# Performance work log

Measured on AMD Instinct MI355X. Metric: run time of the kernel, lower is better.

## Reference

```python
import jax, jax.numpy as jnp
import numpy as np
import math

WIDTH = 1024
NUM_HEADS = 16
HEAD_DIM = WIDTH // NUM_HEADS
WINDOW_SIZE = 256
MIN_LOGITS_VALUE = -1e30


def setup_inputs() -> dict:
    key = jax.random.key(0)
    ks = jax.random.split(key, 7)
    b, t = 2, 2048
    std = math.sqrt(1.0 / WIDTH)
    x = jax.random.normal(ks[0], (b, t, WIDTH), dtype=jnp.float32)
    segment_pos = jnp.broadcast_to(jnp.arange(t, dtype=jnp.int32)[None, :], (b, t))
    Wq = jax.random.normal(ks[1], (WIDTH, WIDTH), dtype=jnp.float32) * std
    Wk = jax.random.normal(ks[2], (HEAD_DIM, WIDTH), dtype=jnp.float32) * std
    Wv = jax.random.normal(ks[3], (HEAD_DIM, WIDTH), dtype=jnp.float32) * std
    Wf = jax.random.normal(ks[4], (WIDTH, WIDTH), dtype=jnp.float32) * std
    bf = jnp.zeros((WIDTH,), dtype=jnp.float32)
    return {"x": x, "segment_pos": segment_pos, "Wq": Wq, "Wk": Wk, "Wv": Wv, "Wf": Wf, "bf": bf}


def reference(x, segment_pos, Wq, Wk, Wv, Wf, bf):
    b, t, _ = x.shape
    # projections (Linear: x @ W.T)
    q = (x @ Wq.T).reshape(b, t, NUM_HEADS, HEAD_DIM)  # [b,t,n,h]
    k = x @ Wk.T  # [b,t,h] single shared KV head (MQA)
    v = x @ Wv.T  # [b,t,h]
    scale = 1.0 / math.sqrt(HEAD_DIM)
    logits = jnp.einsum('btnh,bsh->bnts', q, k) * scale  # [b,n,t,s]
    # sliding-window causal mask: q_pos >= k_pos and q_pos <= k_pos + window
    ar = jnp.arange(t)
    qp = ar[:, None]
    kp = ar[None, :]
    mask = (qp >= kp) & (qp <= kp + WINDOW_SIZE)  # [t,s]
    masked = jnp.where(mask[None, None, :, :], logits, MIN_LOGITS_VALUE)
    probs = jax.nn.softmax(masked.astype(jnp.float32), axis=-1).astype(logits.dtype)
    out = jnp.einsum('bnts,bsh->btnh', probs, v)  # [b,t,n,h]
    out = out.reshape(b, t, WIDTH)
    return out @ Wf.T + bf
```

## Files before the change

kernel.cpp:

```cpp
#include <hip/hip_runtime.h>
#include <stdint.h>

#define B_SZ   2
#define T_SEQ  2048
#define WIDTH_ 1024
#define NH     16
#define HD     64
#define WIN    256
#define MROWS  (B_SZ * T_SEQ)
#define NQKV   1152

typedef __attribute__((ext_vector_type(4))) float f32x4;
typedef __attribute__((ext_vector_type(8))) short s16x8;

typedef __attribute__((address_space(1))) const void gas_void;
typedef __attribute__((address_space(3))) void las_void;

#define MFMA(a, b, c) __builtin_amdgcn_mfma_f32_16x16x32_bf16((a), (b), (c), 0, 0, 0)

__device__ __forceinline__ void gload_lds16(const void* g, void* l) {
  __builtin_amdgcn_global_load_lds((gas_void*)g, (las_void*)l, 16, 0, 0);
}

__device__ __forceinline__ ushort f2bf(float f) {
  union { float f; uint32_t u; } v; v.f = f;
  uint32_t u = v.u;
  return (ushort)((u + 0x7FFFu + ((u >> 16) & 1u)) >> 16);
}

__global__ void prep_kernel(const float* __restrict__ x,
                            const float* __restrict__ Wq,
                            const float* __restrict__ Wk,
                            const float* __restrict__ Wv,
                            const float* __restrict__ Wf,
                            ushort* __restrict__ xb,
                            ushort* __restrict__ wqkv,
                            ushort* __restrict__ wfb) {
  const int XN = MROWS * WIDTH_ / 4;
  const int WQ = NQKV * WIDTH_ / 4;
  const int WF = WIDTH_ * WIDTH_ / 4;
  int i = blockIdx.x * blockDim.x + threadIdx.x;
  float4 v;
  ushort* dst;
  if (i < XN) {
    v = ((const float4*)x)[i];
    dst = xb + i * 4;
  } else if (i < XN + WQ) {
    int j = i - XN;
    int row = (j * 4) >> 10;
    int col = (j * 4) & 1023;
    const float* src = (row < 1024) ? (Wq + row * 1024 + col)
                     : (row < 1088) ? (Wk + (row - 1024) * 1024 + col)
                                    : (Wv + (row - 1088) * 1024 + col);
    v = *(const float4*)src;
    dst = wqkv + j * 4;
  } else if (i < XN + WQ + WF) {
    int j = i - XN - WQ;
    v = ((const float4*)Wf)[j];
    dst = wfb + j * 4;
  } else {
    return;
  }
  ushort4 o;
  o.x = f2bf(v.x); o.y = f2bf(v.y); o.z = f2bf(v.z); o.w = f2bf(v.w);
  *(ushort4*)dst = o;
}

template <int MODE>
__global__ __launch_bounds__(256) void gemm_kernel(
    const ushort* __restrict__ A, const ushort* __restrict__ B,
    ushort* __restrict__ qb, ushort* __restrict__ kb, ushort* __restrict__ vb,
    float* __restrict__ Cf, const float* __restrict__ bias) {
  const int K = 1024;
  const int w = threadIdx.x >> 6;
  const int lane = threadIdx.x & 63;
  const int g = lane >> 4;
  const int r16 = lane & 15;
  const int m0 = blockIdx.y * 128;
  const int n0 = blockIdx.x * 128;
  const int wm = (w >> 1) * 64;
  const int wn = (w & 1) * 64;

  __shared__ ushort As[128 * 32];
  __shared__ ushort Bs[128 * 32];

  f32x4 acc[4][4] = {};

  for (int k0 = 0; k0 < K; k0 += 32) {
#pragma unroll
    for (int i = 0; i < 2; ++i) {
      int c = i * 256 + w * 64 + lane;
      int row = c >> 2;
      int ke = (c & 3) * 8;
      int ldsbase = (i * 256 + w * 64) * 16;
      gload_lds16(A + (size_t)(m0 + row) * K + k0 + ke, (char*)As + ldsbase);
      gload_lds16(B + (size_t)(n0 + row) * K + k0 + ke, (char*)Bs + ldsbase);
    }
    __syncthreads();

    s16x8 af[4], bfr[4];
#pragma unroll
    for (int t = 0; t < 4; ++t) {
      af[t]  = *(const s16x8*)&As[(wm + t * 16 + r16) * 32 + g * 8];
      bfr[t] = *(const s16x8*)&Bs[(wn + t * 16 + r16) * 32 + g * 8];
    }
#pragma unroll
    for (int mb = 0; mb < 4; ++mb)
#pragma unroll
      for (int nb = 0; nb < 4; ++nb)
        acc[mb][nb] = MFMA(af[mb], bfr[nb], acc[mb][nb]);
    __syncthreads();
  }

#pragma unroll
  for (int mb = 0; mb < 4; ++mb)
#pragma unroll
    for (int nb = 0; nb < 4; ++nb) {
      int n = n0 + wn + nb * 16 + r16;
      int mbase = m0 + wm + mb * 16 + 4 * g;
      if (MODE == 0) {
#pragma unroll
        for (int r = 0; r < 4; ++r) {
          ushort h = f2bf(acc[mb][nb][r]);
          int m = mbase + r;
          if (n < 1024)      qb[m * 1024 + n] = h;
          else if (n < 1088) kb[m * 64 + (n - 1024)] = h;
          else               vb[m * 64 + (n - 1088)] = h;
        }
      } else {
        float bv = bias[n];
#pragma unroll
        for (int r = 0; r < 4; ++r)
          Cf[(size_t)(mbase + r) * 1024 + n] = acc[mb][nb][r] + bv;
      }
    }
}

__global__ void vtrans_kernel(const ushort* __restrict__ vb,
                              ushort* __restrict__ vt) {
  int o = blockIdx.x * blockDim.x + threadIdx.x;
  int t = o & 2047;
  int d = (o >> 11) & 63;
  int b = o >> 17;
  vt[o] = vb[(size_t)(b * 2048 + t) * 64 + d];
}

__global__ __launch_bounds__(64) void attn_kernel(
    const ushort* __restrict__ qb, const ushort* __restrict__ kb,
    const ushort* __restrict__ vt, ushort* __restrict__ ao) {
  const int lane = threadIdx.x;
  const int g = lane >> 4;
  const int r16 = lane & 15;
  const int blk = blockIdx.x;
  const int qt = blk & 127;
  const int h = (blk >> 7) & 15;
  const int b = blk >> 11;
  const int q0 = qt * 16;
  const int qp = q0 + r16;

  const ushort* qrow = qb + (size_t)(b * 2048 + qp) * 1024 + h * 64;
  s16x8 qf0 = *(const s16x8*)(qrow + g * 8);
  s16x8 qf1 = *(const s16x8*)(qrow + 32 + g * 8);

  f32x4 oacc[4] = {};
  float mrun = -1e30f, ls = 0.f;

  int kt0 = q0 - WIN;
  if (kt0 < 0) kt0 = 0;
  kt0 &= ~31;

  for (int kt = kt0; kt <= q0; kt += 32) {
    int kr0 = kt + r16;
    int kr1 = kt + 16 + r16;
    if (kr1 > 2047) kr1 = 2047;
    const ushort* kp0 = kb + (size_t)(b * 2048 + kr0) * 64;
    const ushort* kp1 = kb + (size_t)(b * 2048 + kr1) * 64;
    s16x8 k00 = *(const s16x8*)(kp0 + g * 8);
    s16x8 k01 = *(const s16x8*)(kp0 + 32 + g * 8);
    s16x8 k10 = *(const s16x8*)(kp1 + g * 8);
    s16x8 k11 = *(const s16x8*)(kp1 + 32 + g * 8);

    f32x4 s0 = {}, s1 = {};
    s0 = MFMA(k00, qf0, s0);
    s0 = MFMA(k01, qf1, s0);
    s1 = MFMA(k10, qf0, s1);
    s1 = MFMA(k11, qf1, s1);

    float p0[4], p1[4];
    float tm = -1e30f;
#pragma unroll
    for (int r = 0; r < 4; ++r) {
      int ka = kt + 4 * g + r;
      int kb2 = ka + 16;
      float v0 = (ka <= qp && qp - ka <= WIN) ? s0[r] * 0.125f : -1e30f;
      float v1 = (kb2 <= qp && qp - kb2 <= WIN) ? s1[r] * 0.125f : -1e30f;
      p0[r] = v0; p1[r] = v1;
      tm = fmaxf(tm, fmaxf(v0, v1));
    }
    tm = fmaxf(tm, __shfl_xor(tm, 16));
    tm = fmaxf(tm, __shfl_xor(tm, 32));

    float mnew = fmaxf(mrun, tm);
    float corr = __expf(mrun - mnew);
    float ts = 0.f;
    s16x8 pf;
#pragma unroll
    for (int r = 0; r < 4; ++r) {
      float e0 = __expf(p0[r] - mnew);
      float e1 = __expf(p1[r] - mnew);
      ts += e0 + e1;
      pf[r] = (short)f2bf(e0);
      pf[4 + r] = (short)f2bf(e1);
    }
    ts += __shfl_xor(ts, 16);
    ts += __shfl_xor(ts, 32);
    ls = ls * corr + ts;
    mrun = mnew;

#pragma unroll
    for (int db = 0; db < 4; ++db) oacc[db] *= corr;

#pragma unroll
    for (int db = 0; db < 4; ++db) {
      const ushort* vrow = vt + (size_t)(b * 64 + db * 16 + r16) * 2048 + kt;
      ushort4 va = *(const ushort4*)(vrow + 4 * g);
      ushort4 vc = *(const ushort4*)(vrow + 16 + 4 * g);
      s16x8 vf;
      vf[0] = (short)va.x; vf[1] = (short)va.y; vf[2] = (short)va.z; vf[3] = (short)va.w;
      vf[4] = (short)vc.x; vf[5] = (short)vc.y; vf[6] = (short)vc.z; vf[7] = (short)vc.w;
      oacc[db] = MFMA(vf, pf, oacc[db]);
    }
  }

  float inv = 1.0f / ls;
  ushort* orow = ao + (size_t)(b * 2048 + qp) * 1024 + h * 64;
#pragma unroll
  for (int db = 0; db < 4; ++db) {
    ushort4 o;
    o.x = f2bf(oacc[db][0] * inv);
    o.y = f2bf(oacc[db][1] * inv);
    o.z = f2bf(oacc[db][2] * inv);
    o.w = f2bf(oacc[db][3] * inv);
    *(ushort4*)(orow + db * 16 + 4 * g) = o;
  }
}

extern "C" void kernel_launch(void* const* d_in, const int* in_sizes, int n_in,
                              void* d_out, int out_size, void* d_ws, size_t ws_size,
                              hipStream_t stream) {
  const float* x  = (const float*)d_in[0];
  const float* Wq = (const float*)d_in[2];
  const float* Wk = (const float*)d_in[3];
  const float* Wv = (const float*)d_in[4];
  const float* Wf = (const float*)d_in[5];
  const float* bf = (const float*)d_in[6];
  float* out = (float*)d_out;

  uint8_t* w8 = (uint8_t*)d_ws;
  ushort* xb   = (ushort*)(w8 + 0);
  ushort* qbuf = (ushort*)(w8 + 8388608);
  ushort* attn = (ushort*)(w8 + 16777216);
  ushort* wqkv = (ushort*)(w8 + 25165824);
  ushort* wfb  = (ushort*)(w8 + 27525120);
  ushort* vt   = (ushort*)(w8 + 29622272);
  ushort* kbuf = (ushort*)(w8 + 30146560);
  ushort* vbuf = (ushort*)(w8 + 30670848);

  prep_kernel<<<6272, 256, 0, stream>>>(x, Wq, Wk, Wv, Wf, xb, wqkv, wfb);
  gemm_kernel<0><<<dim3(9, 32), 256, 0, stream>>>(xb, wqkv, qbuf, kbuf, vbuf,
                                                  nullptr, nullptr);
  vtrans_kernel<<<1024, 256, 0, stream>>>(vbuf, vt);
  attn_kernel<<<4096, 64, 0, stream>>>(qbuf, kbuf, vt, attn);
  gemm_kernel<1><<<dim3(8, 32), 256, 0, stream>>>(attn, wfb, nullptr, nullptr,
                                                  nullptr, out, bf);
}
```

Before: 187.0 us.

## Double-buffer GEMM LDS, fuse V transpose into epilogue, widen attention to 32 queries

The GEMM kernel now double-buffers its LDS tiles, so the global-to-LDS loads for the next K slice are issued while the current slice is being computed. The QKV GEMM epilogue writes V directly in transposed layout, which removes the separate vtrans kernel launch and its extra pass over V. Each attention block now handles 32 queries instead of 16, so K and V fragments loaded once are shared across two query groups, and the next K tile is prefetched into registers. In exchange, LDS use doubles, attention register pressure rises, the transposed V stores in the epilogue are strided, and the attention grid is halved, which lowers occupancy.

```diff
diff --git a/kernel.cpp b/kernel.cpp
--- a/kernel.cpp
+++ b/kernel.cpp
@@ -66,12 +66,39 @@
   *(ushort4*)dst = o;
 }
 
+#define G_STAGE(AS, BS, KOFF) do {                                          \
+  _Pragma("unroll")                                                         \
+  for (int i_ = 0; i_ < 2; ++i_) {                                          \
+    int c_ = i_ * 256 + w * 64 + lane;                                      \
+    int row_ = c_ >> 2;                                                     \
+    int ke_ = (c_ & 3) * 8;                                                 \
+    int ldsb_ = (i_ * 256 + w * 64) * 16;                                   \
+    gload_lds16(A + (size_t)(m0 + row_) * 1024 + (KOFF) + ke_,              \
+                (char*)(AS) + ldsb_);                                       \
+    gload_lds16(B + (size_t)(n0 + row_) * 1024 + (KOFF) + ke_,              \
+                (char*)(BS) + ldsb_);                                       \
+  }                                                                         \
+} while (0)
+
+#define G_COMPUTE(AS, BS) do {                                              \
+  s16x8 af_[4], bf_[4];                                                     \
+  _Pragma("unroll")                                                         \
+  for (int t_ = 0; t_ < 4; ++t_) {                                          \
+    af_[t_] = *(const s16x8*)&(AS)[(wm + t_ * 16 + r16) * 32 + g * 8];      \
+    bf_[t_] = *(const s16x8*)&(BS)[(wn + t_ * 16 + r16) * 32 + g * 8];      \
+  }                                                                         \
+  _Pragma("unroll")                                                         \
+  for (int mb_ = 0; mb_ < 4; ++mb_)                                         \
+    _Pragma("unroll")                                                       \
+    for (int nb_ = 0; nb_ < 4; ++nb_)                                       \
+      acc[mb_][nb_] = MFMA(af_[mb_], bf_[nb_], acc[mb_][nb_]);              \
+} while (0)
+
 template <int MODE>
 __global__ __launch_bounds__(256) void gemm_kernel(
     const ushort* __restrict__ A, const ushort* __restrict__ B,
-    ushort* __restrict__ qb, ushort* __restrict__ kb, ushort* __restrict__ vb,
+    ushort* __restrict__ qb, ushort* __restrict__ kb, ushort* __restrict__ vt,
     float* __restrict__ Cf, const float* __restrict__ bias) {
-  const int K = 1024;
   const int w = threadIdx.x >> 6;
   const int lane = threadIdx.x & 63;
   const int g = lane >> 4;
@@ -81,35 +108,21 @@
   const int wm = (w >> 1) * 64;
   const int wn = (w & 1) * 64;
 
-  __shared__ ushort As[128 * 32];
-  __shared__ ushort Bs[128 * 32];
+  __shared__ ushort As0[128 * 32];
+  __shared__ ushort Bs0[128 * 32];
+  __shared__ ushort As1[128 * 32];
+  __shared__ ushort Bs1[128 * 32];
 
   f32x4 acc[4][4] = {};
 
-  for (int k0 = 0; k0 < K; k0 += 32) {
-#pragma unroll
-    for (int i = 0; i < 2; ++i) {
-      int c = i * 256 + w * 64 + lane;
-      int row = c >> 2;
-      int ke = (c & 3) * 8;
-      int ldsbase = (i * 256 + w * 64) * 16;
-      gload_lds16(A + (size_t)(m0 + row) * K + k0 + ke, (char*)As + ldsbase);
-      gload_lds16(B + (size_t)(n0 + row) * K + k0 + ke, (char*)Bs + ldsbase);
-    }
+  G_STAGE(As0, Bs0, 0);
+  for (int k0 = 0; k0 < 1024; k0 += 64) {
     __syncthreads();
-
-    s16x8 af[4], bfr[4];
-#pragma unroll
-    for (int t = 0; t < 4; ++t) {
-      af[t]  = *(const s16x8*)&As[(wm + t * 16 + r16) * 32 + g * 8];
-      bfr[t] = *(const s16x8*)&Bs[(wn + t * 16 + r16) * 32 + g * 8];
-    }
-#pragma unroll
-    for (int mb = 0; mb < 4; ++mb)
-#pragma unroll
-      for (int nb = 0; nb < 4; ++nb)
-        acc[mb][nb] = MFMA(af[mb], bfr[nb], acc[mb][nb]);
+    G_STAGE(As1, Bs1, k0 + 32);
+    G_COMPUTE(As0, Bs0);
     __syncthreads();
+    if (k0 + 64 < 1024) G_STAGE(As0, Bs0, k0 + 64);
+    G_COMPUTE(As1, Bs1);
   }
 
 #pragma unroll
@@ -125,7 +138,8 @@
           int m = mbase + r;
           if (n < 1024)      qb[m * 1024 + n] = h;
           else if (n < 1088) kb[m * 64 + (n - 1024)] = h;
-          else               vb[m * 64 + (n - 1088)] = h;
+          else               vt[((size_t)((m >> 11) * 64 + (n - 1088))) * 2048 +
+                                (m & 2047)] = h;
         }
       } else {
         float bv = bias[n];
@@ -134,15 +148,6 @@
           Cf[(size_t)(mbase + r) * 1024 + n] = acc[mb][nb][r] + bv;
       }
     }
-}
-
-__global__ void vtrans_kernel(const ushort* __restrict__ vb,
-                              ushort* __restrict__ vt) {
-  int o = blockIdx.x * blockDim.x + threadIdx.x;
-  int t = o & 2047;
-  int d = (o >> 11) & 63;
-  int b = o >> 17;
-  vt[o] = vb[(size_t)(b * 2048 + t) * 64 + d];
 }
 
 __global__ __launch_bounds__(64) void attn_kernel(
@@ -152,73 +157,94 @@
   const int g = lane >> 4;
   const int r16 = lane & 15;
   const int blk = blockIdx.x;
-  const int qt = blk & 127;
-  const int h = (blk >> 7) & 15;
-  const int b = blk >> 11;
-  const int q0 = qt * 16;
-  const int qp = q0 + r16;
-
-  const ushort* qrow = qb + (size_t)(b * 2048 + qp) * 1024 + h * 64;
-  s16x8 qf0 = *(const s16x8*)(qrow + g * 8);
-  s16x8 qf1 = *(const s16x8*)(qrow + 32 + g * 8);
-
-  f32x4 oacc[4] = {};
-  float mrun = -1e30f, ls = 0.f;
+  const int qt = blk & 63;
+  const int h = (blk >> 6) & 15;
+  const int b = blk >> 10;
+  const int q0 = qt * 32;
+  const int qpA = q0 + r16;
+  const int qpB = q0 + 16 + r16;
+
+  const ushort* qrowA = qb + (size_t)(b * 2048 + qpA) * 1024 + h * 64;
+  const ushort* qrowB = qb + (size_t)(b * 2048 + qpB) * 1024 + h * 64;
+  s16x8 qfA0 = *(const s16x8*)(qrowA + g * 8);
+  s16x8 qfA1 = *(const s16x8*)(qrowA + 32 + g * 8);
+  s16x8 qfB0 = *(const s16x8*)(qrowB + g * 8);
+  s16x8 qfB1 = *(const s16x8*)(qrowB + 32 + g * 8);
+
+  f32x4 oaccA[4] = {}, oaccB[4] = {};
+  float mA = -1e30f, lA = 0.f, mB = -1e30f, lB = 0.f;
 
   int kt0 = q0 - WIN;
   if (kt0 < 0) kt0 = 0;
   kt0 &= ~31;
 
+  s16x8 k00, k01, k10, k11;
+  {
+    const ushort* kp0 = kb + (size_t)(b * 2048 + kt0 + r16) * 64;
+    const ushort* kp1 = kb + (size_t)(b * 2048 + kt0 + 16 + r16) * 64;
+    k00 = *(const s16x8*)(kp0 + g * 8);
+    k01 = *(const s16x8*)(kp0 + 32 + g * 8);
+    k10 = *(const s16x8*)(kp1 + g * 8);
+    k11 = *(const s16x8*)(kp1 + 32 + g * 8);
+  }
+
   for (int kt = kt0; kt <= q0; kt += 32) {
-    int kr0 = kt + r16;
-    int kr1 = kt + 16 + r16;
-    if (kr1 > 2047) kr1 = 2047;
-    const ushort* kp0 = kb + (size_t)(b * 2048 + kr0) * 64;
-    const ushort* kp1 = kb + (size_t)(b * 2048 + kr1) * 64;
-    s16x8 k00 = *(const s16x8*)(kp0 + g * 8);
-    s16x8 k01 = *(const s16x8*)(kp0 + 32 + g * 8);
-    s16x8 k10 = *(const s16x8*)(kp1 + g * 8);
-    s16x8 k11 = *(const s16x8*)(kp1 + 32 + g * 8);
-
-    f32x4 s0 = {}, s1 = {};
-    s0 = MFMA(k00, qf0, s0);
-    s0 = MFMA(k01, qf1, s0);
-    s1 = MFMA(k10, qf0, s1);
-    s1 = MFMA(k11, qf1, s1);
-
-    float p0[4], p1[4];
-    float tm = -1e30f;
+    s16x8 c00 = k00, c01 = k01, c10 = k10, c11 = k11;
+    if (kt + 32 <= q0) {
+      const ushort* kp0 = kb + (size_t)(b * 2048 + kt + 32 + r16) * 64;
+      const ushort* kp1 = kb + (size_t)(b * 2048 + kt + 48 + r16) * 64;
+      k00 = *(const s16x8*)(kp0 + g * 8);
+      k01 = *(const s16x8*)(kp0 + 32 + g * 8);
+      k10 = *(const s16x8*)(kp1 + g * 8);
+      k11 = *(const s16x8*)(kp1 + 32 + g * 8);
+    }
+
+    f32x4 sA0 = {}, sA1 = {}, sB0 = {}, sB1 = {};
+    sA0 = MFMA(c00, qfA0, sA0); sA0 = MFMA(c01, qfA1, sA0);
+    sA1 = MFMA(c10, qfA0, sA1); sA1 = MFMA(c11, qfA1, sA1);
+    sB0 = MFMA(c00, qfB0, sB0); sB0 = MFMA(c01, qfB1, sB0);
+    sB1 = MFMA(c10, qfB0, sB1); sB1 = MFMA(c11, qfB1, sB1);
+
+    float pA0[4], pA1[4], pB0[4], pB1[4];
+    float tmA = -1e30f, tmB = -1e30f;
 #pragma unroll
     for (int r = 0; r < 4; ++r) {
       int ka = kt + 4 * g + r;
-      int kb2 = ka + 16;
-      float v0 = (ka <= qp && qp - ka <= WIN) ? s0[r] * 0.125f : -1e30f;
-      float v1 = (kb2 <= qp && qp - kb2 <= WIN) ? s1[r] * 0.125f : -1e30f;
-      p0[r] = v0; p1[r] = v1;
-      tm = fmaxf(tm, fmaxf(v0, v1));
-    }
-    tm = fmaxf(tm, __shfl_xor(tm, 16));
-    tm = fmaxf(tm, __shfl_xor(tm, 32));
-
-    float mnew = fmaxf(mrun, tm);
-    float corr = __expf(mrun - mnew);
-    float ts = 0.f;
-    s16x8 pf;
+      int kc = ka + 16;
+      float a0 = (ka <= qpA && qpA - ka <= WIN) ? sA0[r] * 0.125f : -1e30f;
+      float a1 = (kc <= qpA && qpA - kc <= WIN) ? sA1[r] * 0.125f : -1e30f;
+      float b0 = (ka <= qpB && qpB - ka <= WIN) ? sB0[r] * 0.125f : -1e30f;
+      float b1 = (kc <= qpB && qpB - kc <= WIN) ? sB1[r] * 0.125f : -1e30f;
+      pA0[r] = a0; pA1[r] = a1; pB0[r] = b0; pB1[r] = b1;
+      tmA = fmaxf(tmA, fmaxf(a0, a1));
+      tmB = fmaxf(tmB, fmaxf(b0, b1));
+    }
+    tmA = fmaxf(tmA, __shfl_xor(tmA, 16));
+    tmA = fmaxf(tmA, __shfl_xor(tmA, 32));
+    tmB = fmaxf(tmB, __shfl_xor(tmB, 16));
+    tmB = fmaxf(tmB, __shfl_xor(tmB, 32));
+
+    float mnA = fmaxf(mA, tmA), mnB = fmaxf(mB, tmB);
+    float corrA = __expf(mA - mnA), corrB = __expf(mB - mnB);
+    float tsA = 0.f, tsB = 0.f;
+    s16x8 pfA, pfB;
 #pragma unroll
     for (int r = 0; r < 4; ++r) {
-      float e0 = __expf(p0[r] - mnew);
-      float e1 = __expf(p1[r] - mnew);
-      ts += e0 + e1;
-      pf[r] = (short)f2bf(e0);
-      pf[4 + r] = (short)f2bf(e1);
-    }
-    ts += __shfl_xor(ts, 16);
-    ts += __shfl_xor(ts, 32);
-    ls = ls * corr + ts;
-    mrun = mnew;
-
-#pragma unroll
-    for (int db = 0; db < 4; ++db) oacc[db] *= corr;
+      float eA0 = __expf(pA0[r] - mnA);
+      float eA1 = __expf(pA1[r] - mnA);
+      float eB0 = __expf(pB0[r] - mnB);
+      float eB1 = __expf(pB1[r] - mnB);
+      tsA += eA0 + eA1; tsB += eB0 + eB1;
+      pfA[r] = (short)f2bf(eA0); pfA[4 + r] = (short)f2bf(eA1);
+      pfB[r] = (short)f2bf(eB0); pfB[4 + r] = (short)f2bf(eB1);
+    }
+    tsA += __shfl_xor(tsA, 16); tsA += __shfl_xor(tsA, 32);
+    tsB += __shfl_xor(tsB, 16); tsB += __shfl_xor(tsB, 32);
+    lA = lA * corrA + tsA; mA = mnA;
+    lB = lB * corrB + tsB; mB = mnB;
+
+#pragma unroll
+    for (int db = 0; db < 4; ++db) { oaccA[db] *= corrA; oaccB[db] *= corrB; }
 
 #pragma unroll
     for (int db = 0; db < 4; ++db) {
@@ -228,20 +254,23 @@
       s16x8 vf;
       vf[0] = (short)va.x; vf[1] = (short)va.y; vf[2] = (short)va.z; vf[3] = (short)va.w;
       vf[4] = (short)vc.x; vf[5] = (short)vc.y; vf[6] = (short)vc.z; vf[7] = (short)vc.w;
-      oacc[db] = MFMA(vf, pf, oacc[db]);
-    }
-  }
-
-  float inv = 1.0f / ls;
-  ushort* orow = ao + (size_t)(b * 2048 + qp) * 1024 + h * 64;
+      oaccA[db] = MFMA(vf, pfA, oaccA[db]);
+      oaccB[db] = MFMA(vf, pfB, oaccB[db]);
+    }
+  }
+
+  float invA = 1.0f / lA, invB = 1.0f / lB;
+  ushort* orowA = ao + (size_t)(b * 2048 + qpA) * 1024 + h * 64;
+  ushort* orowB = ao + (size_t)(b * 2048 + qpB) * 1024 + h * 64;
 #pragma unroll
   for (int db = 0; db < 4; ++db) {
-    ushort4 o;
-    o.x = f2bf(oacc[db][0] * inv);
-    o.y = f2bf(oacc[db][1] * inv);
-    o.z = f2bf(oacc[db][2] * inv);
-    o.w = f2bf(oacc[db][3] * inv);
-    *(ushort4*)(orow + db * 16 + 4 * g) = o;
+    ushort4 oA, oB;
+    oA.x = f2bf(oaccA[db][0] * invA); oA.y = f2bf(oaccA[db][1] * invA);
+    oA.z = f2bf(oaccA[db][2] * invA); oA.w = f2bf(oaccA[db][3] * invA);
+    oB.x = f2bf(oaccB[db][0] * invB); oB.y = f2bf(oaccB[db][1] * invB);
+    oB.z = f2bf(oaccB[db][2] * invB); oB.w = f2bf(oaccB[db][3] * invB);
+    *(ushort4*)(orowA + db * 16 + 4 * g) = oA;
+    *(ushort4*)(orowB + db * 16 + 4 * g) = oB;
   }
 }
 
@@ -262,15 +291,13 @@
   ushort* attn = (ushort*)(w8 + 16777216);
   ushort* wqkv = (ushort*)(w8 + 25165824);
   ushort* wfb  = (ushort*)(w8 + 27525120);
-  ushort* vt   = (ushort*)(w8 + 29622272);
-  ushort* kbuf = (ushort*)(w8 + 30146560);
-  ushort* vbuf = (ushort*)(w8 + 30670848);
+  ushort* kbuf = (ushort*)(w8 + 29622272);
+  ushort* vt   = (ushort*)(w8 + 30146560);
 
   prep_kernel<<<6272, 256, 0, stream>>>(x, Wq, Wk, Wv, Wf, xb, wqkv, wfb);
-  gemm_kernel<0><<<dim3(9, 32), 256, 0, stream>>>(xb, wqkv, qbuf, kbuf, vbuf,
+  gemm_kernel<0><<<dim3(9, 32), 256, 0, stream>>>(xb, wqkv, qbuf, kbuf, vt,
                                                   nullptr, nullptr);
-  vtrans_kernel<<<1024, 256, 0, stream>>>(vbuf, vt);
-  attn_kernel<<<4096, 64, 0, stream>>>(qbuf, kbuf, vt, attn);
+  attn_kernel<<<2048, 64, 0, stream>>>(qbuf, kbuf, vt, attn);
   gemm_kernel<1><<<dim3(8, 32), 256, 0, stream>>>(attn, wfb, nullptr, nullptr,
                                                   nullptr, out, bf);
 }
```

New measurement: 158.6 us. 15.2% less time.
